# Performance work log

Hardware: AMD Instinct MI355X
Metric: run time of the kernel (lower is better)

The kernel has to match this reference:

```python
import jax, jax.numpy as jnp
import numpy as np

L, D, N = 4096, 1024, 16  # seq_len, d_model, hiddens_per_input


def setup_inputs() -> dict:
    key = jax.random.key(0)
    ks = jax.random.split(key, 9)
    x = jax.random.normal(ks[0], (L, D), dtype=jnp.float32)
    # Delta param (pre-softplus); softplus(Delta) > 0 is the discretization step
    Delta = jax.random.normal(ks[1], (D,), dtype=jnp.float32)
    # A stored as (re, im); default scheme uses A_re = -1 (stable), theta in [0, 2pi)
    A_re = -(0.5 + 0.5 * jax.random.uniform(ks[2], (D, N), dtype=jnp.float32))
    A_im = jax.random.uniform(ks[3], (D, N), dtype=jnp.float32) * 2.0 * jnp.pi
    scale = 1.0 / jnp.sqrt(jnp.float32(D))  # matrix_init: randn / sqrt(shape[0])
    B_re = jax.random.normal(ks[4], (D, N), dtype=jnp.float32) * scale
    B_im = jax.random.normal(ks[5], (D, N), dtype=jnp.float32) * scale
    C_re = jax.random.normal(ks[6], (D, N), dtype=jnp.float32) * scale
    C_im = jax.random.normal(ks[7], (D, N), dtype=jnp.float32) * scale
    D_param = jax.random.normal(ks[8], (D,), dtype=jnp.float32) * scale
    return {"x": x, "Delta": Delta, "A_re": A_re, "A_im": A_im,
            "B_re": B_re, "B_im": B_im, "C_re": C_re, "C_im": C_im,
            "D_param": D_param}


def _binary_operator_diag(q_i, q_j):
    """Associative op for diagonal linear recurrence h_j = A_j h_{j-1} + b_j."""
    A_i, b_i = q_i
    A_j, b_j = q_j
    return (A_j * A_i, A_j * b_i + b_j)


def reference(x, Delta, A_re, A_im, B_re, B_im, C_re, C_im, D_param):
    Bc = B_re + 1j * B_im                      # (D, N) complex
    Cc = C_re + 1j * C_im                      # (D, N) complex
    Ac = A_re + 1j * A_im                      # (D, N) complex
    dt = jax.nn.softplus(Delta)                # (D,)
    # shared_Delta=True branch: Lambda = exp(dt[:, None] * A), repeated over L
    Lam = jnp.exp(dt[:, None] * Ac)            # (D, N) complex
    Lambda_elements = jnp.broadcast_to(Lam[None, :, :], (x.shape[0], *Lam.shape))
    # Bu = einsum('D, D N, L D -> L D N', dt, B, x)
    Bu_elements = jnp.einsum('D,DN,LD->LDN', dt.astype(Bc.dtype), Bc,
                             x.astype(Bc.dtype))
    _, hidden_states = jax.lax.associative_scan(
        _binary_operator_diag, (Lambda_elements, Bu_elements))  # (L, D, N)
    out = jnp.einsum('LDN,DN->LD', hidden_states, Cc) + D_param[None, :] * x
    return out.real
```

## Files before the change

### kernel.cpp

```cpp
#include <hip/hip_runtime.h>
#include <math.h>

constexpr int L   = 4096;
constexpr int D   = 1024;
constexpr int N   = 16;
constexpr int CPB = 4;
constexpr int NB  = D / CPB;
constexpr int NCB = 128;
constexpr int T   = L / NCB;
constexpr int NT  = 1024;

typedef float v2 __attribute__((ext_vector_type(2)));

__device__ __forceinline__ float softplus_f(float v) {
    return fmaxf(v, 0.0f) + log1pf(expf(-fabsf(v)));
}

__device__ __forceinline__ void lam_fast(float ar, float ai, float dt,
                                         float& lr, float& li) {
    float e = __expf(ar * dt);
    float s, c;
    __sincosf(ai * dt, &s, &c);
    lr = e * c;
    li = e * s;
}

__device__ __forceinline__ v2 vfma(v2 a, v2 b, v2 c) {
    return __builtin_elementwise_fma(a, b, c);
}

__global__ __launch_bounds__(NT, 4) void k_fused(
    const float* __restrict__ x,
    const float* __restrict__ Delta,
    const float* __restrict__ A_re, const float* __restrict__ A_im,
    const float* __restrict__ B_re, const float* __restrict__ B_im,
    const float* __restrict__ C_re, const float* __restrict__ C_im,
    const float* __restrict__ Dp,
    float* __restrict__ out)
{
    __shared__ float  xs[T * 512];
    __shared__ float2 sums[NCB * 64];

    const int b  = blockIdx.x;
    const int d0 = (b & 7) * 128 + (b >> 3) * 4;
    const int t  = threadIdx.x;

    {
        const int sct = t & 127;
        const int si  = t >> 7;
        float4 v[4];
        #pragma unroll
        for (int k = 0; k < 4; ++k) {
            int l = sct * T + si * 4 + k;
            v[k] = *(const float4*)(x + (size_t)l * D + d0);
        }
        #pragma unroll
        for (int k = 0; k < 4; ++k)
            *(float4*)&xs[(si * 4 + k) * 512 + sct * 4] = v[k];
    }

    const int h  = t & 1;
    const int dd = (t >> 1) & 3;
    const int ct = t >> 3;
    const int d  = d0 + dd;
    const float dt = softplus_f(Delta[d]);

    v2 LR[4], LI[4];
    {
        const int base = d * N + h * 8;
        float4 a0 = *(const float4*)(A_re + base);
        float4 a1 = *(const float4*)(A_re + base + 4);
        float4 m0 = *(const float4*)(A_im + base);
        float4 m1 = *(const float4*)(A_im + base + 4);
        const float ar[8] = {a0.x, a0.y, a0.z, a0.w, a1.x, a1.y, a1.z, a1.w};
        const float ai[8] = {m0.x, m0.y, m0.z, m0.w, m1.x, m1.y, m1.z, m1.w};
        #pragma unroll
        for (int p = 0; p < 4; ++p) {
            float lr0, li0, lr1, li1;
            lam_fast(ar[2 * p], ai[2 * p], dt, lr0, li0);
            lam_fast(ar[2 * p + 1], ai[2 * p + 1], dt, lr1, li1);
            LR[p] = (v2){lr0, lr1};
            LI[p] = (v2){li0, li1};
        }
    }
    __syncthreads();

    v2 GR[4] = {(v2)0, (v2)0, (v2)0, (v2)0};
    v2 GI[4] = {(v2)0, (v2)0, (v2)0, (v2)0};
    #pragma unroll 4
    for (int i = 0; i < T; ++i) {
        float xv = xs[i * 512 + ct * 4 + dd];
        v2 XV = (v2){xv, xv};
        #pragma unroll
        for (int p = 0; p < 4; ++p) {
            v2 t2 = vfma(-LI[p], GI[p], XV);
            v2 nr = vfma(LR[p], GR[p], t2);
            GI[p] = vfma(LR[p], GI[p], LI[p] * GR[p]);
            GR[p] = nr;
        }
    }
    {
        float2* sp = &sums[ct * 64 + dd * 16 + h * 8];
        #pragma unroll
        for (int p = 0; p < 4; ++p) {
            sp[2 * p]     = make_float2(GR[p].x, GI[p].x);
            sp[2 * p + 1] = make_float2(GR[p].y, GI[p].y);
        }
    }
    __syncthreads();

    if (t < 64) {
        const int dd2 = t >> 4, n2 = t & 15;
        const int d2  = d0 + dd2;
        const float dt2 = softplus_f(Delta[d2]);
        float lr, li;
        lam_fast(A_re[d2 * N + n2], A_im[d2 * N + n2], dt2, lr, li);
        #pragma unroll
        for (int k = 0; k < 5; ++k) {
            float nr = lr * lr - li * li;
            li = 2.0f * lr * li;
            lr = nr;
        }
        float cr = 0.0f, ci = 0.0f;
        #pragma unroll
        for (int c0 = 0; c0 < NCB; c0 += 16) {
            float2 sv[16];
            #pragma unroll
            for (int u = 0; u < 16; ++u) sv[u] = sums[(c0 + u) * 64 + t];
            #pragma unroll
            for (int u = 0; u < 16; ++u) {
                sums[(c0 + u) * 64 + t] = make_float2(cr, ci);
                float nr = fmaf(lr, cr, fmaf(-li, ci, sv[u].x));
                ci = fmaf(lr, ci, fmaf(li, cr, sv[u].y));
                cr = nr;
            }
        }
    }

    v2 CR[4], CI[4];
    {
        const int base = d * N + h * 8;
        float4 b0 = *(const float4*)(B_re + base);
        float4 b1 = *(const float4*)(B_re + base + 4);
        float4 e0 = *(const float4*)(B_im + base);
        float4 e1 = *(const float4*)(B_im + base + 4);
        float4 f0 = *(const float4*)(C_re + base);
        float4 f1 = *(const float4*)(C_re + base + 4);
        float4 g0 = *(const float4*)(C_im + base);
        float4 g1 = *(const float4*)(C_im + base + 4);
        const float br[8] = {b0.x, b0.y, b0.z, b0.w, b1.x, b1.y, b1.z, b1.w};
        const float bi[8] = {e0.x, e0.y, e0.z, e0.w, e1.x, e1.y, e1.z, e1.w};
        const float cr[8] = {f0.x, f0.y, f0.z, f0.w, f1.x, f1.y, f1.z, f1.w};
        const float ci[8] = {g0.x, g0.y, g0.z, g0.w, g1.x, g1.y, g1.z, g1.w};
        #pragma unroll
        for (int p = 0; p < 4; ++p) {
            CR[p] = (v2){dt * (cr[2*p] * br[2*p] - ci[2*p] * bi[2*p]),
                         dt * (cr[2*p+1] * br[2*p+1] - ci[2*p+1] * bi[2*p+1])};
            CI[p] = (v2){dt * (cr[2*p] * bi[2*p] + ci[2*p] * br[2*p]),
                         dt * (cr[2*p+1] * bi[2*p+1] + ci[2*p+1] * br[2*p+1])};
        }
    }
    const float dpv = Dp[d];
    __syncthreads();

    {
        const float2* cp = &sums[ct * 64 + dd * 16 + h * 8];
        #pragma unroll
        for (int p = 0; p < 4; ++p) {
            float2 c0 = cp[2 * p], c1 = cp[2 * p + 1];
            GR[p] = (v2){c0.x, c1.x};
            GI[p] = (v2){c0.y, c1.y};
        }
    }
    #pragma unroll
    for (int ob = 0; ob < T / 8; ++ob) {
        float Vh[4];
        #pragma unroll
        for (int ib = 0; ib < 4; ++ib) {
            #pragma unroll
            for (int u = 0; u < 2; ++u) {
                int i = ob * 8 + ib * 2 + u;
                float xv = xs[i * 512 + ct * 4 + dd];
                v2 XV = (v2){xv, xv};
                v2 ACC = (v2)0;
                #pragma unroll
                for (int p = 0; p < 4; ++p) {
                    v2 t2 = vfma(-LI[p], GI[p], XV);
                    v2 nr = vfma(LR[p], GR[p], t2);
                    GI[p] = vfma(LR[p], GI[p], LI[p] * GR[p]);
                    GR[p] = nr;
                    ACC = vfma(CR[p], GR[p], ACC);
                    ACC = vfma(-CI[p], GI[p], ACC);
                }
                float acc = ACC.x + ACC.y;
                acc += __shfl_xor(acc, 1);
                acc = fmaf(dpv, xv, acc);
                if (u == h) Vh[ib] = acc;
            }
        }
        float f[4];
        f[dd]     = Vh[dd];
        f[dd ^ 1] = __shfl_xor(Vh[dd ^ 1], 2);
        f[dd ^ 2] = __shfl_xor(Vh[dd ^ 2], 4);
        f[dd ^ 3] = __shfl_xor(Vh[dd ^ 3], 6);
        int row = ct * T + ob * 8 + dd * 2 + h;
        *(float4*)(out + (size_t)row * D + d0) =
            make_float4(f[0], f[1], f[2], f[3]);
    }
}

extern "C" void kernel_launch(void* const* d_in, const int* in_sizes, int n_in,
                              void* d_out, int out_size, void* d_ws, size_t ws_size,
                              hipStream_t stream) {
    const float* x     = (const float*)d_in[0];
    const float* Delta = (const float*)d_in[1];
    const float* A_re  = (const float*)d_in[2];
    const float* A_im  = (const float*)d_in[3];
    const float* B_re  = (const float*)d_in[4];
    const float* B_im  = (const float*)d_in[5];
    const float* C_re  = (const float*)d_in[6];
    const float* C_im  = (const float*)d_in[7];
    const float* Dp    = (const float*)d_in[8];
    float* out = (float*)d_out;

    k_fused<<<NB, NT, 0, stream>>>(x, Delta, A_re, A_im, B_re, B_im,
                                   C_re, C_im, Dp, out);
}
```

Before: 104.6 us.

## Parallelize cross-chunk carry scan across all waves with two-level hierarchy

The serial 128-step carry scan over chunk sums, run by a single wave, is replaced by a two-level scan. Each of 16 waves scans 8 chunks, one wave scans the 16 wave totals using Lambda^256, and all waves then fix up their chunks. The sums array is padded to 65 per row to reduce LDS bank conflicts. The B/C/D parameter loads are hoisted earlier to overlap with the scan. This shortens the critical path while the other 15 waves would otherwise idle, at the cost of two extra barriers and a little more LDS.

Result: no change. 103.2 us (-1.4%).

```diff
diff --git a/kernel.cpp b/kernel.cpp
--- a/kernel.cpp
+++ b/kernel.cpp
@@ -9,6 +9,7 @@
 constexpr int NCB = 128;
 constexpr int T   = L / NCB;
 constexpr int NT  = 1024;
+constexpr int PAD = 65;
 
 typedef float v2 __attribute__((ext_vector_type(2)));
 
@@ -39,7 +40,8 @@
     float* __restrict__ out)
 {
     __shared__ float  xs[T * 512];
-    __shared__ float2 sums[NCB * 64];
+    __shared__ float2 sums[NCB * PAD];
+    __shared__ float2 tot[16 * 64];
 
     const int b  = blockIdx.x;
     const int d0 = (b & 7) * 128 + (b >> 3) * 4;
@@ -100,7 +102,7 @@
         }
     }
     {
-        float2* sp = &sums[ct * 64 + dd * 16 + h * 8];
+        float2* sp = &sums[ct * PAD + dd * 16 + h * 8];
         #pragma unroll
         for (int p = 0; p < 4; ++p) {
             sp[2 * p]     = make_float2(GR[p].x, GI[p].x);
@@ -109,45 +111,86 @@
     }
     __syncthreads();
 
-    if (t < 64) {
-        const int dd2 = t >> 4, n2 = t & 15;
+    const int lane = t & 63;
+    const int w    = t >> 6;
+    float l32r, l32i;
+    {
+        const int dd2 = lane >> 4, n2 = lane & 15;
         const int d2  = d0 + dd2;
         const float dt2 = softplus_f(Delta[d2]);
-        float lr, li;
-        lam_fast(A_re[d2 * N + n2], A_im[d2 * N + n2], dt2, lr, li);
+        lam_fast(A_re[d2 * N + n2], A_im[d2 * N + n2], dt2, l32r, l32i);
         #pragma unroll
         for (int k = 0; k < 5; ++k) {
-            float nr = lr * lr - li * li;
-            li = 2.0f * lr * li;
-            lr = nr;
-        }
+            float nr = l32r * l32r - l32i * l32i;
+            l32i = 2.0f * l32r * l32i;
+            l32r = nr;
+        }
+    }
+    {
         float cr = 0.0f, ci = 0.0f;
         #pragma unroll
-        for (int c0 = 0; c0 < NCB; c0 += 16) {
-            float2 sv[16];
-            #pragma unroll
-            for (int u = 0; u < 16; ++u) sv[u] = sums[(c0 + u) * 64 + t];
-            #pragma unroll
-            for (int u = 0; u < 16; ++u) {
-                sums[(c0 + u) * 64 + t] = make_float2(cr, ci);
-                float nr = fmaf(lr, cr, fmaf(-li, ci, sv[u].x));
-                ci = fmaf(lr, ci, fmaf(li, cr, sv[u].y));
-                cr = nr;
-            }
+        for (int k = 0; k < 8; ++k) {
+            const int idx = (w * 8 + k) * PAD + lane;
+            float2 sv = sums[idx];
+            sums[idx] = make_float2(cr, ci);
+            float nr = fmaf(l32r, cr, fmaf(-l32i, ci, sv.x));
+            ci = fmaf(l32r, ci, fmaf(l32i, cr, sv.y));
+            cr = nr;
+        }
+        tot[w * 64 + lane] = make_float2(cr, ci);
+    }
+    __syncthreads();
+
+    float4 b0, b1, e0, e1, f0, f1, g0, g1;
+    {
+        const int base = d * N + h * 8;
+        b0 = *(const float4*)(B_re + base);
+        b1 = *(const float4*)(B_re + base + 4);
+        e0 = *(const float4*)(B_im + base);
+        e1 = *(const float4*)(B_im + base + 4);
+        f0 = *(const float4*)(C_re + base);
+        f1 = *(const float4*)(C_re + base + 4);
+        g0 = *(const float4*)(C_im + base);
+        g1 = *(const float4*)(C_im + base + 4);
+    }
+    const float dpv = Dp[d];
+
+    if (t < 64) {
+        float rr = l32r, ri = l32i;
+        #pragma unroll
+        for (int k = 0; k < 3; ++k) {
+            float nr = rr * rr - ri * ri;
+            ri = 2.0f * rr * ri;
+            rr = nr;
+        }
+        float cr = 0.0f, ci = 0.0f;
+        #pragma unroll
+        for (int u = 0; u < 16; ++u) {
+            float2 sv = tot[u * 64 + t];
+            tot[u * 64 + t] = make_float2(cr, ci);
+            float nr = fmaf(rr, cr, fmaf(-ri, ci, sv.x));
+            ci = fmaf(rr, ci, fmaf(ri, cr, sv.y));
+            cr = nr;
+        }
+    }
+    __syncthreads();
+
+    {
+        float2 g = tot[w * 64 + lane];
+        float gr = g.x, gi = g.y;
+        #pragma unroll
+        for (int k = 0; k < 8; ++k) {
+            const int idx = (w * 8 + k) * PAD + lane;
+            float2 p = sums[idx];
+            sums[idx] = make_float2(gr + p.x, gi + p.y);
+            float nr = l32r * gr - l32i * gi;
+            gi = fmaf(l32r, gi, l32i * gr);
+            gr = nr;
         }
     }
 
     v2 CR[4], CI[4];
     {
-        const int base = d * N + h * 8;
-        float4 b0 = *(const float4*)(B_re + base);
-        float4 b1 = *(const float4*)(B_re + base + 4);
-        float4 e0 = *(const float4*)(B_im + base);
-        float4 e1 = *(const float4*)(B_im + base + 4);
-        float4 f0 = *(const float4*)(C_re + base);
-        float4 f1 = *(const float4*)(C_re + base + 4);
-        float4 g0 = *(const float4*)(C_im + base);
-        float4 g1 = *(const float4*)(C_im + base + 4);
         const float br[8] = {b0.x, b0.y, b0.z, b0.w, b1.x, b1.y, b1.z, b1.w};
         const float bi[8] = {e0.x, e0.y, e0.z, e0.w, e1.x, e1.y, e1.z, e1.w};
         const float cr[8] = {f0.x, f0.y, f0.z, f0.w, f1.x, f1.y, f1.z, f1.w};
@@ -160,11 +203,10 @@
                          dt * (cr[2*p+1] * bi[2*p+1] + ci[2*p+1] * br[2*p+1])};
         }
     }
-    const float dpv = Dp[d];
-    __syncthreads();
-
-    {
-        const float2* cp = &sums[ct * 64 + dd * 16 + h * 8];
+    __syncthreads();
+
+    {
+        const float2* cp = &sums[ct * PAD + dd * 16 + h * 8];
         #pragma unroll
         for (int p = 0; p < 4; ++p) {
             float2 c0 = cp[2 * p], c1 = cp[2 * p + 1];
```
